# Performance work log

Hardware: AMD Instinct MI355X
Metric: run time of the kernel (lower is better)

The kernel has to match this reference:

```python
import jax, jax.numpy as jnp
import numpy as np

B, S, D, H, L, O = 64, 512, 512, 1024, 2, 1000


def setup_inputs() -> dict:
    key = jax.random.key(0)
    ks = jax.random.split(key, 12)
    s = 0.05
    return {
        "x": jax.random.normal(ks[0], (B, S, D), jnp.float32),
        "h0": jnp.zeros((L, B, H), jnp.float32),
        "c0": jnp.zeros((L, B, H), jnp.float32),
        "W_ih0": jax.random.normal(ks[1], (4 * H, D), jnp.float32) * s,
        "W_hh0": jax.random.normal(ks[2], (4 * H, H), jnp.float32) * s,
        "b_ih0": jax.random.normal(ks[3], (4 * H,), jnp.float32) * s,
        "b_hh0": jax.random.normal(ks[4], (4 * H,), jnp.float32) * s,
        "W_ih1": jax.random.normal(ks[5], (4 * H, H), jnp.float32) * s,
        "W_hh1": jax.random.normal(ks[6], (4 * H, H), jnp.float32) * s,
        "b_ih1": jax.random.normal(ks[7], (4 * H,), jnp.float32) * s,
        "b_hh1": jax.random.normal(ks[8], (4 * H,), jnp.float32) * s,
        "W_fc": jax.random.normal(ks[9], (O, H), jnp.float32) * s,
        "b_fc": jax.random.normal(ks[10], (O,), jnp.float32) * s,
    }


def _lstm_cell(x_t, h, c, W_ih, W_hh, b_ih, b_hh):
    # standard LSTMCell: fused 4-gate GEMM, gate order (i, f, g, o)
    gates = x_t @ W_ih.T + b_ih + h @ W_hh.T + b_hh  # [B, 4H]
    i, f, g, o = jnp.split(gates, 4, axis=-1)
    i = jax.nn.sigmoid(i)
    f = jax.nn.sigmoid(f)
    g = jnp.tanh(g)
    o = jax.nn.sigmoid(o)
    c_new = f * c + i * g
    h_new = o * jnp.tanh(c_new)
    return h_new, c_new


def reference(x, h0, c0, W_ih0, W_hh0, b_ih0, b_hh0, W_ih1, W_hh1, b_ih1, b_hh1, W_fc, b_fc):
    params = [(W_ih0, W_hh0, b_ih0, b_hh0), (W_ih1, W_hh1, b_ih1, b_hh1)]

    def step(carry, x_t):
        hs, cs = carry  # tuples of [B,H] per layer
        new_h, new_c = [], []
        inp = x_t
        for l in range(L):  # fixed small layer count
            h_l, c_l = _lstm_cell(inp, hs[l], cs[l], *params[l])
            new_h.append(h_l)
            new_c.append(c_l)
            inp = h_l
        return (tuple(new_h), tuple(new_c)), None

    xs = jnp.swapaxes(x, 0, 1)  # [S, B, D]
    init = (tuple(h0[l] for l in range(L)), tuple(c0[l] for l in range(L)))
    (hs, _), _ = jax.lax.scan(step, init, xs)
    # dropout is inference-mode identity; output_activation=None
    out = hs[-1] @ W_fc.T + b_fc  # [B, O]
    return out
```

## Files before the change

kernel.cpp:

```cpp
#include <hip/hip_runtime.h>

#define B_ 64
#define S_ 512
#define D_ 512
#define H_ 1024

typedef __attribute__((ext_vector_type(8))) short bf16x8;
typedef __attribute__((ext_vector_type(4))) float f32x4;
typedef unsigned short u16;
typedef unsigned int u32;

#define MFMA(a, b, c) __builtin_amdgcn_mfma_f32_16x16x32_bf16(a, b, c, 0, 0, 0)

__device__ __forceinline__ u16 f2bf(float f) {
    u32 u = __float_as_uint(f);
    u += 0x7fffu + ((u >> 16) & 1u);
    return (u16)(u >> 16);
}
__device__ __forceinline__ float sigm(float x) { return 1.0f / (1.0f + __expf(-x)); }
__device__ __forceinline__ float tanh_f(float x) { return 1.0f - 2.0f / (__expf(2.0f * x) + 1.0f); }

__device__ __forceinline__ bf16x8 cvt8(const float* p) {
    float4 f0 = ((const float4*)p)[0];
    float4 f1 = ((const float4*)p)[1];
    bf16x8 v;
    v[0] = (short)f2bf(f0.x); v[1] = (short)f2bf(f0.y);
    v[2] = (short)f2bf(f0.z); v[3] = (short)f2bf(f0.w);
    v[4] = (short)f2bf(f1.x); v[5] = (short)f2bf(f1.y);
    v[6] = (short)f2bf(f1.z); v[7] = (short)f2bf(f1.w);
    return v;
}

__device__ __forceinline__ void llc_ld(bf16x8& d, const u16* p) {
    asm volatile("global_load_dwordx4 %0, %1, off sc0 sc1" : "=v"(d) : "v"(p));
}
__device__ __forceinline__ void vm0() {
    asm volatile("s_waitcnt vmcnt(0)" ::: "memory");
}
__device__ __forceinline__ void fence_frag(bf16x8& d) {
    asm volatile("" : "+v"(d));
}
__device__ __forceinline__ void llc_st16(u16* p, u16 v) {
    u32 vv = v;
    asm volatile("global_store_short %0, %1, off sc0 sc1" :: "v"(p), "v"(vv) : "memory");
}

__global__ void prep_w(const float* __restrict__ Wih, const float* __restrict__ Whh,
                       u16* __restrict__ Wc, int Kx, int Kw, int total8) {
    int idx = blockIdx.x * 256 + threadIdx.x;
    if (idx >= total8) return;
    int kc8 = Kw >> 3;
    int n = idx / kc8;
    int kc = (idx - n * kc8) << 3;
    const float* src = (kc < Kx) ? (Wih + (size_t)n * Kx + kc)
                                 : (Whh + (size_t)n * (Kw - Kx) + (kc - Kx));
    *(bf16x8*)(Wc + (size_t)n * Kw + kc) = cvt8(src);
}

__global__ void prep_misc2(const float* __restrict__ h0in,
                           const float* __restrict__ bih0, const float* __restrict__ bhh0,
                           const float* __restrict__ bih1, const float* __restrict__ bhh1,
                           float* __restrict__ bias0, float* __restrict__ bias1,
                           u16* __restrict__ h0a, u16* __restrict__ h0b,
                           u16* __restrict__ h1a, u16* __restrict__ h1b,
                           int* __restrict__ bar) {
    int idx = blockIdx.x * 256 + threadIdx.x;
    if (idx < 1024) bar[idx] = 0;
    if (idx < 4096) { bias0[idx] = bih0[idx] + bhh0[idx]; return; }
    if (idx < 8192) { int i = idx - 4096; bias1[i] = bih1[i] + bhh1[i]; return; }
    int r = idx - 8192;
    if (r >= 2 * B_ * H_) return;
    int l = r >> 16;
    int rr = r & 65535;
    u16 hb = f2bf(h0in[r]);
    if (l == 0) { h0a[rr] = hb; h0b[rr] = hb; }
    else        { h1a[rr] = hb; h1b[rr] = hb; }
}

__global__ __launch_bounds__(512, 2) void lstm_persist(
    const float* __restrict__ x,
    const u16* __restrict__ W0c, const u16* __restrict__ W1c,
    const float* __restrict__ bias0, const float* __restrict__ bias1,
    const float* __restrict__ c0in,
    u16* __restrict__ h0a, u16* __restrict__ h0b,
    u16* __restrict__ h1a, u16* __restrict__ h1b,
    float* __restrict__ h1f,
    int* __restrict__ bar) {
    const int bk = blockIdx.x;
    const int cgp = bk >> 1;
    const int mh = bk & 1;
    const int tid = threadIdx.x;
    const int w = tid >> 6;
    const int lane = tid & 63;
    const int quad = lane >> 4;
    const int l16 = lane & 15;

    int gc[2];
    #pragma unroll
    for (int n = 0; n < 2; ++n) {
        int c = n * 16 + l16;
        gc[n] = (c >> 3) * 1024 + cgp * 8 + (c & 7);
    }

    bf16x8 w0x[2][2], w0h[2][4];
    bf16x8 w1f[2][8];
    #pragma unroll
    for (int n = 0; n < 2; ++n) {
        #pragma unroll
        for (int kf = 0; kf < 2; ++kf)
            w0x[n][kf] = *(const bf16x8*)(W0c + (size_t)gc[n] * 1536 + w * 64 + kf * 32 + quad * 8);
        #pragma unroll
        for (int kf = 0; kf < 4; ++kf)
            w0h[n][kf] = *(const bf16x8*)(W0c + (size_t)gc[n] * 1536 + 512 + w * 128 + kf * 32 + quad * 8);
        #pragma unroll
        for (int kf = 0; kf < 8; ++kf)
            w1f[n][kf] = *(const bf16x8*)(W1c + (size_t)gc[n] * 2048 + w * 256 + kf * 32 + quad * 8);
    }

    __shared__ float part[8 * 32 * 37];
    __shared__ float c0l[256], c1l[256];
    __shared__ float b0l[32], b1l[32];

    if (tid < 32) {
        int gg = tid >> 3, j = tid & 7;
        b0l[tid] = bias0[gg * 1024 + cgp * 8 + j];
        b1l[tid] = bias1[gg * 1024 + cgp * 8 + j];
    }
    if (tid < 256) {
        int b = tid >> 3, j = tid & 7;
        int gi = (mh * 32 + b) * 1024 + cgp * 8 + j;
        c0l[tid] = c0in[gi];
        c1l[tid] = c0in[65536 + gi];
    }
    __syncthreads();

    const int brow0 = mh * 32 + l16;
    const int brow1 = brow0 + 16;

    f32x4 xacc[2][2];
    #define XPART(t)                                                                 \
        {                                                                            \
            xacc[0][0] = (f32x4){0.f,0.f,0.f,0.f}; xacc[0][1] = (f32x4){0.f,0.f,0.f,0.f}; \
            xacc[1][0] = (f32x4){0.f,0.f,0.f,0.f}; xacc[1][1] = (f32x4){0.f,0.f,0.f,0.f}; \
            _Pragma("unroll")                                                        \
            for (int kf = 0; kf < 2; ++kf) {                                         \
                int k = w * 64 + kf * 32 + quad * 8;                                 \
                bf16x8 a0 = cvt8(x + (size_t)brow0 * 262144 + (t) * 512 + k);        \
                bf16x8 a1 = cvt8(x + (size_t)brow1 * 262144 + (t) * 512 + k);        \
                xacc[0][0] = MFMA(a0, w0x[0][kf], xacc[0][0]);                       \
                xacc[0][1] = MFMA(a0, w0x[1][kf], xacc[0][1]);                       \
                xacc[1][0] = MFMA(a1, w0x[0][kf], xacc[1][0]);                       \
                xacc[1][1] = MFMA(a1, w0x[1][kf], xacc[1][1]);                       \
            }                                                                        \
        }

    XPART(0);

    for (int p = 0; p <= S_; ++p) {
        const int rd = p & 1;
        const u16* h0r = rd ? h0b : h0a;
        u16*       h0w_ = rd ? h0a : h0b;
        const u16* h1r = rd ? h1b : h1a;
        u16*       h1w_ = rd ? h1a : h1b;

        if (p > 0) {
            if (tid == 0) {
                int target = 256 * p;
                for (int it = 0; it < 20000; ++it) {
                    if (__hip_atomic_load(&bar[0], __ATOMIC_RELAXED, __HIP_MEMORY_SCOPE_AGENT) >= target)
                        break;
                    __builtin_amdgcn_s_sleep(1);
                }
            }
            __syncthreads();
        }

        bf16x8 a0[4], a1[4];
        if (p < S_) {
            #pragma unroll
            for (int kf = 0; kf < 4; ++kf) {
                int ko = w * 128 + kf * 32 + quad * 8;
                llc_ld(a0[kf], h0r + brow0 * 1024 + ko);
                llc_ld(a1[kf], h0r + brow1 * 1024 + ko);
            }
            vm0();
            #pragma unroll
            for (int kf = 0; kf < 4; ++kf) { fence_frag(a0[kf]); fence_frag(a1[kf]); }
        }
        bf16x8 pb0[8], pb1[8];
        if (p >= 1) {
            #pragma unroll
            for (int kf = 0; kf < 8; ++kf) {
                int k = w * 256 + kf * 32;
                const u16* src = (k < 1024) ? h0r : h1r;
                int ko = (k & 1023) + quad * 8;
                llc_ld(pb0[kf], src + brow0 * 1024 + ko);
                llc_ld(pb1[kf], src + brow1 * 1024 + ko);
            }
        }

        if (p < S_) {
            f32x4 acc00 = xacc[0][0], acc01 = xacc[0][1];
            f32x4 acc10 = xacc[1][0], acc11 = xacc[1][1];
            #pragma unroll
            for (int kf = 0; kf < 4; ++kf) {
                acc00 = MFMA(a0[kf], w0h[0][kf], acc00);
                acc01 = MFMA(a0[kf], w0h[1][kf], acc01);
                acc10 = MFMA(a1[kf], w0h[0][kf], acc10);
                acc11 = MFMA(a1[kf], w0h[1][kf], acc11);
            }
            #pragma unroll
            for (int r = 0; r < 4; ++r) {
                int r0 = quad * 4 + r, r1 = 16 + quad * 4 + r;
                part[w * 1184 + r0 * 37 + l16]      = acc00[r];
                part[w * 1184 + r0 * 37 + 16 + l16] = acc01[r];
                part[w * 1184 + r1 * 37 + l16]      = acc10[r];
                part[w * 1184 + r1 * 37 + 16 + l16] = acc11[r];
            }
            __syncthreads();
            if (tid < 256) {
                int b = tid >> 3, j = tid & 7;
                float g4[4];
                #pragma unroll
                for (int gg = 0; gg < 4; ++gg) {
                    float s = b0l[gg * 8 + j];
                    #pragma unroll
                    for (int w8 = 0; w8 < 8; ++w8)
                        s += part[w8 * 1184 + b * 37 + gg * 8 + j];
                    g4[gg] = s;
                }
                float c = c0l[tid];
                float cn = sigm(g4[1]) * c + sigm(g4[0]) * tanh_f(g4[2]);
                float hn = sigm(g4[3]) * tanh_f(cn);
                c0l[tid] = cn;
                llc_st16(h0w_ + (mh * 32 + b) * 1024 + cgp * 8 + j, f2bf(hn));
            }
            __syncthreads();
        }

        if (p >= 1) {
            vm0();
            #pragma unroll
            for (int kf = 0; kf < 8; ++kf) { fence_frag(pb0[kf]); fence_frag(pb1[kf]); }
            f32x4 acc00 = {0.f,0.f,0.f,0.f}, acc01 = {0.f,0.f,0.f,0.f};
            f32x4 acc10 = {0.f,0.f,0.f,0.f}, acc11 = {0.f,0.f,0.f,0.f};
            #pragma unroll
            for (int kf = 0; kf < 8; ++kf) {
                acc00 = MFMA(pb0[kf], w1f[0][kf], acc00);
                acc01 = MFMA(pb0[kf], w1f[1][kf], acc01);
                acc10 = MFMA(pb1[kf], w1f[0][kf], acc10);
                acc11 = MFMA(pb1[kf], w1f[1][kf], acc11);
            }
            #pragma unroll
            for (int r = 0; r < 4; ++r) {
                int r0 = quad * 4 + r, r1 = 16 + quad * 4 + r;
                part[w * 1184 + r0 * 37 + l16]      = acc00[r];
                part[w * 1184 + r0 * 37 + 16 + l16] = acc01[r];
                part[w * 1184 + r1 * 37 + l16]      = acc10[r];
                part[w * 1184 + r1 * 37 + 16 + l16] = acc11[r];
            }
            __syncthreads();
            if (tid < 256) {
                int b = tid >> 3, j = tid & 7;
                float g4[4];
                #pragma unroll
                for (int gg = 0; gg < 4; ++gg) {
                    float s = b1l[gg * 8 + j];
                    #pragma unroll
                    for (int w8 = 0; w8 < 8; ++w8)
                        s += part[w8 * 1184 + b * 37 + gg * 8 + j];
                    g4[gg] = s;
                }
                float c = c1l[tid];
                float cn = sigm(g4[1]) * c + sigm(g4[0]) * tanh_f(g4[2]);
                float hn = sigm(g4[3]) * tanh_f(cn);
                c1l[tid] = cn;
                int gi = (mh * 32 + b) * 1024 + cgp * 8 + j;
                llc_st16(h1w_ + gi, f2bf(hn));
                if (p == S_) h1f[gi] = hn;
            }
            __syncthreads();
        }

        if (p < S_) {
            if (tid == 0)
                __hip_atomic_fetch_add(&bar[0], 1, __ATOMIC_RELAXED, __HIP_MEMORY_SCOPE_AGENT);
            if (p + 1 < S_) XPART(p + 1);
        }
    }
}

__global__ void fc_k(const float* __restrict__ h1f, const float* __restrict__ Wfc,
                     const float* __restrict__ bfc, float* __restrict__ out) {
    int idx = blockIdx.x * 256 + threadIdx.x;
    if (idx >= 64 * 1000) return;
    int o = idx % 1000;
    int b = idx / 1000;
    const float4* hr = (const float4*)(h1f + b * H_);
    const float4* wr = (const float4*)(Wfc + (size_t)o * H_);
    float s = 0.f;
    #pragma unroll 4
    for (int k = 0; k < 256; ++k) {
        float4 a = hr[k];
        float4 w = wr[k];
        s += a.x * w.x + a.y * w.y + a.z * w.z + a.w * w.w;
    }
    out[idx] = s + bfc[o];
}

extern "C" void kernel_launch(void* const* d_in, const int* in_sizes, int n_in,
                              void* d_out, int out_size, void* d_ws, size_t ws_size,
                              hipStream_t stream) {
    const float* x    = (const float*)d_in[0];
    const float* h0in = (const float*)d_in[1];
    const float* c0in = (const float*)d_in[2];
    const float* Wih0 = (const float*)d_in[3];
    const float* Whh0 = (const float*)d_in[4];
    const float* bih0 = (const float*)d_in[5];
    const float* bhh0 = (const float*)d_in[6];
    const float* Wih1 = (const float*)d_in[7];
    const float* Whh1 = (const float*)d_in[8];
    const float* bih1 = (const float*)d_in[9];
    const float* bhh1 = (const float*)d_in[10];
    const float* Wfc  = (const float*)d_in[11];
    const float* bfc  = (const float*)d_in[12];
    float* out = (float*)d_out;

    char* ws = (char*)d_ws;
    size_t off = 0;
    auto alloc = [&](size_t bytes) {
        void* p = ws + off;
        off += (bytes + 255) & ~(size_t)255;
        return p;
    };
    u16* W0c   = (u16*)alloc((size_t)4096 * 1536 * 2);
    u16* W1c   = (u16*)alloc((size_t)4096 * 2048 * 2);
    float* bias0 = (float*)alloc(4096 * 4);
    float* bias1 = (float*)alloc(4096 * 4);
    u16* h0A   = (u16*)alloc(B_ * H_ * 2);
    u16* h0B   = (u16*)alloc(B_ * H_ * 2);
    u16* h1A   = (u16*)alloc(B_ * H_ * 2);
    u16* h1B   = (u16*)alloc(B_ * H_ * 2);
    float* h1f = (float*)alloc(B_ * H_ * 4);
    int* bar   = (int*)alloc(4096);

    prep_w<<<786432 / 256, 256, 0, stream>>>(Wih0, Whh0, W0c, 512, 1536, 786432);
    prep_w<<<1048576 / 256, 256, 0, stream>>>(Wih1, Whh1, W1c, 1024, 2048, 1048576);
    prep_misc2<<<(8192 + 2 * B_ * H_ + 255) / 256, 256, 0, stream>>>(
        h0in, bih0, bhh0, bih1, bhh1, bias0, bias1, h0A, h0B, h1A, h1B, bar);

    void* args[] = {(void*)&x, (void*)&W0c, (void*)&W1c, (void*)&bias0, (void*)&bias1,
                    (void*)&c0in, (void*)&h0A, (void*)&h0B, (void*)&h1A, (void*)&h1B,
                    (void*)&h1f, (void*)&bar};
    hipLaunchCooperativeKernel((void*)lstm_persist, dim3(256), dim3(512), args, 0, stream);

    fc_k<<<(64000 + 255) / 256, 256, 0, stream>>>(h1f, Wfc, bfc, out);
}
```

Before: 5.886 ms.

## Replace global atomic barrier with per-block flags and overlap layer phases

Replaces the single global atomic counter barrier with per-block step flags: each block writes its own flag and waits only on the flags of the producer blocks it reads from, polled by a whole wavefront. The layer-0 and layer-1 gate reductions get separate shared buffers, which drops a couple of __syncthreads per step, and the h loads for both layers are waited on together with vmcnt. The shared-memory layout is changed so the gate reduction reads float4 vectors, with bias stored gate-interleaved. The goal is lower per-step synchronization latency across the 512 sequential steps. The risks are ordering and visibility bugs in the flag protocol and correctness of the partial vmcnt wait.

```diff
diff --git a/kernel.cpp b/kernel.cpp
--- a/kernel.cpp
+++ b/kernel.cpp
@@ -37,12 +37,24 @@
 __device__ __forceinline__ void vm0() {
     asm volatile("s_waitcnt vmcnt(0)" ::: "memory");
 }
+__device__ __forceinline__ void vmw16() {
+    asm volatile("s_waitcnt vmcnt(16)" ::: "memory");
+}
 __device__ __forceinline__ void fence_frag(bf16x8& d) {
     asm volatile("" : "+v"(d));
 }
 __device__ __forceinline__ void llc_st16(u16* p, u16 v) {
     u32 vv = v;
     asm volatile("global_store_short %0, %1, off sc0 sc1" :: "v"(p), "v"(vv) : "memory");
+}
+__device__ __forceinline__ void llc_st32(int* p, int v) {
+    asm volatile("global_store_dword %0, %1, off sc0 sc1" :: "v"(p), "v"(v) : "memory");
+}
+__device__ __forceinline__ void llc_ld2(int& a, int& b, const int* p0, const int* p1) {
+    asm volatile("global_load_dword %0, %2, off sc0 sc1\n"
+                 "global_load_dword %1, %3, off sc0 sc1\n"
+                 "s_waitcnt vmcnt(0)"
+                 : "=&v"(a), "=&v"(b) : "v"(p0), "v"(p1) : "memory");
 }
 
 __global__ void prep_w(const float* __restrict__ Wih, const float* __restrict__ Whh,
@@ -65,7 +77,7 @@
                            u16* __restrict__ h1a, u16* __restrict__ h1b,
                            int* __restrict__ bar) {
     int idx = blockIdx.x * 256 + threadIdx.x;
-    if (idx < 1024) bar[idx] = 0;
+    if (idx < 8192) bar[idx] = 0;
     if (idx < 4096) { bias0[idx] = bih0[idx] + bhh0[idx]; return; }
     if (idx < 8192) { int i = idx - 4096; bias1[i] = bih1[i] + bhh1[i]; return; }
     int r = idx - 8192;
@@ -117,14 +129,15 @@
             w1f[n][kf] = *(const bf16x8*)(W1c + (size_t)gc[n] * 2048 + w * 256 + kf * 32 + quad * 8);
     }
 
-    __shared__ float part[8 * 32 * 37];
+    __shared__ __align__(16) float partA[8 * 32 * 36];
+    __shared__ __align__(16) float partB[8 * 32 * 36];
     __shared__ float c0l[256], c1l[256];
-    __shared__ float b0l[32], b1l[32];
+    __shared__ __align__(16) float b0l[32], b1l[32];
 
     if (tid < 32) {
         int gg = tid >> 3, j = tid & 7;
-        b0l[tid] = bias0[gg * 1024 + cgp * 8 + j];
-        b1l[tid] = bias1[gg * 1024 + cgp * 8 + j];
+        b0l[j * 4 + gg] = bias0[gg * 1024 + cgp * 8 + j];
+        b1l[j * 4 + gg] = bias1[gg * 1024 + cgp * 8 + j];
     }
     if (tid < 256) {
         int b = tid >> 3, j = tid & 7;
@@ -136,6 +149,11 @@
 
     const int brow0 = mh * 32 + l16;
     const int brow1 = brow0 + 16;
+
+    const int* q0 = bar + (2 * lane + mh) * 32;
+    const int* q1 = bar + (2 * (lane + 64) + mh) * 32;
+    const int co0 = (l16 & 7) * 4 + (l16 >> 3);
+    const int co1 = co0 + 2;
 
     f32x4 xacc[2][2];
     #define XPART(t)                                                                 \
@@ -164,18 +182,14 @@
         u16*       h1w_ = rd ? h1a : h1b;
 
         if (p > 0) {
-            if (tid == 0) {
-                int target = 256 * p;
-                for (int it = 0; it < 20000; ++it) {
-                    if (__hip_atomic_load(&bar[0], __ATOMIC_RELAXED, __HIP_MEMORY_SCOPE_AGENT) >= target)
-                        break;
-                    __builtin_amdgcn_s_sleep(1);
-                }
-            }
-            __syncthreads();
-        }
-
-        bf16x8 a0[4], a1[4];
+            int f0, f1;
+            for (int it = 0; it < 40000; ++it) {
+                llc_ld2(f0, f1, q0, q1);
+                if (__all((f0 >= p) && (f1 >= p))) break;
+            }
+        }
+
+        bf16x8 a0[4], a1[4], pb0[8], pb1[8];
         if (p < S_) {
             #pragma unroll
             for (int kf = 0; kf < 4; ++kf) {
@@ -183,11 +197,7 @@
                 llc_ld(a0[kf], h0r + brow0 * 1024 + ko);
                 llc_ld(a1[kf], h0r + brow1 * 1024 + ko);
             }
-            vm0();
-            #pragma unroll
-            for (int kf = 0; kf < 4; ++kf) { fence_frag(a0[kf]); fence_frag(a1[kf]); }
-        }
-        bf16x8 pb0[8], pb1[8];
+        }
         if (p >= 1) {
             #pragma unroll
             for (int kf = 0; kf < 8; ++kf) {
@@ -200,6 +210,9 @@
         }
 
         if (p < S_) {
+            if (p >= 1) vmw16(); else vm0();
+            #pragma unroll
+            for (int kf = 0; kf < 4; ++kf) { fence_frag(a0[kf]); fence_frag(a1[kf]); }
             f32x4 acc00 = xacc[0][0], acc01 = xacc[0][1];
             f32x4 acc10 = xacc[1][0], acc11 = xacc[1][1];
             #pragma unroll
@@ -211,37 +224,35 @@
             }
             #pragma unroll
             for (int r = 0; r < 4; ++r) {
-                int r0 = quad * 4 + r, r1 = 16 + quad * 4 + r;
-                part[w * 1184 + r0 * 37 + l16]      = acc00[r];
-                part[w * 1184 + r0 * 37 + 16 + l16] = acc01[r];
-                part[w * 1184 + r1 * 37 + l16]      = acc10[r];
-                part[w * 1184 + r1 * 37 + 16 + l16] = acc11[r];
-            }
-            __syncthreads();
-            if (tid < 256) {
-                int b = tid >> 3, j = tid & 7;
-                float g4[4];
-                #pragma unroll
-                for (int gg = 0; gg < 4; ++gg) {
-                    float s = b0l[gg * 8 + j];
-                    #pragma unroll
-                    for (int w8 = 0; w8 < 8; ++w8)
-                        s += part[w8 * 1184 + b * 37 + gg * 8 + j];
-                    g4[gg] = s;
-                }
-                float c = c0l[tid];
-                float cn = sigm(g4[1]) * c + sigm(g4[0]) * tanh_f(g4[2]);
-                float hn = sigm(g4[3]) * tanh_f(cn);
-                c0l[tid] = cn;
-                llc_st16(h0w_ + (mh * 32 + b) * 1024 + cgp * 8 + j, f2bf(hn));
-            }
-            __syncthreads();
-        }
+                int b0 = quad * 4 + r, b1 = b0 + 16;
+                partA[w * 1152 + b0 * 36 + co0] = acc00[r];
+                partA[w * 1152 + b0 * 36 + co1] = acc01[r];
+                partA[w * 1152 + b1 * 36 + co0] = acc10[r];
+                partA[w * 1152 + b1 * 36 + co1] = acc11[r];
+            }
+        }
+        __syncthreads();
 
         if (p >= 1) {
             vm0();
             #pragma unroll
             for (int kf = 0; kf < 8; ++kf) { fence_frag(pb0[kf]); fence_frag(pb1[kf]); }
+        }
+
+        if (p < S_ && tid < 256) {
+            int b = tid >> 3, j = tid & 7;
+            f32x4 s = *(const f32x4*)&b0l[j * 4];
+            #pragma unroll
+            for (int w8 = 0; w8 < 8; ++w8)
+                s += *(const f32x4*)&partA[w8 * 1152 + b * 36 + j * 4];
+            float c = c0l[tid];
+            float cn = sigm(s[1]) * c + sigm(s[0]) * tanh_f(s[2]);
+            float hn = sigm(s[3]) * tanh_f(cn);
+            c0l[tid] = cn;
+            llc_st16(h0w_ + (mh * 32 + b) * 1024 + cgp * 8 + j, f2bf(hn));
+        }
+
+        if (p >= 1) {
             f32x4 acc00 = {0.f,0.f,0.f,0.f}, acc01 = {0.f,0.f,0.f,0.f};
             f32x4 acc10 = {0.f,0.f,0.f,0.f}, acc11 = {0.f,0.f,0.f,0.f};
             #pragma unroll
@@ -253,38 +264,33 @@
             }
             #pragma unroll
             for (int r = 0; r < 4; ++r) {
-                int r0 = quad * 4 + r, r1 = 16 + quad * 4 + r;
-                part[w * 1184 + r0 * 37 + l16]      = acc00[r];
-                part[w * 1184 + r0 * 37 + 16 + l16] = acc01[r];
-                part[w * 1184 + r1 * 37 + l16]      = acc10[r];
-                part[w * 1184 + r1 * 37 + 16 + l16] = acc11[r];
-            }
+                int b0 = quad * 4 + r, b1 = b0 + 16;
+                partB[w * 1152 + b0 * 36 + co0] = acc00[r];
+                partB[w * 1152 + b0 * 36 + co1] = acc01[r];
+                partB[w * 1152 + b1 * 36 + co0] = acc10[r];
+                partB[w * 1152 + b1 * 36 + co1] = acc11[r];
+            }
+        }
+        __syncthreads();
+        if (p >= 1 && tid < 256) {
+            int b = tid >> 3, j = tid & 7;
+            f32x4 s = *(const f32x4*)&b1l[j * 4];
+            #pragma unroll
+            for (int w8 = 0; w8 < 8; ++w8)
+                s += *(const f32x4*)&partB[w8 * 1152 + b * 36 + j * 4];
+            float c = c1l[tid];
+            float cn = sigm(s[1]) * c + sigm(s[0]) * tanh_f(s[2]);
+            float hn = sigm(s[3]) * tanh_f(cn);
+            c1l[tid] = cn;
+            int gi = (mh * 32 + b) * 1024 + cgp * 8 + j;
+            llc_st16(h1w_ + gi, f2bf(hn));
+            if (p == S_) h1f[gi] = hn;
+        }
+
+        if (p < S_) {
+            vm0();
             __syncthreads();
-            if (tid < 256) {
-                int b = tid >> 3, j = tid & 7;
-                float g4[4];
-                #pragma unroll
-                for (int gg = 0; gg < 4; ++gg) {
-                    float s = b1l[gg * 8 + j];
-                    #pragma unroll
-                    for (int w8 = 0; w8 < 8; ++w8)
-                        s += part[w8 * 1184 + b * 37 + gg * 8 + j];
-                    g4[gg] = s;
-                }
-                float c = c1l[tid];
-                float cn = sigm(g4[1]) * c + sigm(g4[0]) * tanh_f(g4[2]);
-                float hn = sigm(g4[3]) * tanh_f(cn);
-                c1l[tid] = cn;
-                int gi = (mh * 32 + b) * 1024 + cgp * 8 + j;
-                llc_st16(h1w_ + gi, f2bf(hn));
-                if (p == S_) h1f[gi] = hn;
-            }
-            __syncthreads();
-        }
-
-        if (p < S_) {
-            if (tid == 0)
-                __hip_atomic_fetch_add(&bar[0], 1, __ATOMIC_RELAXED, __HIP_MEMORY_SCOPE_AGENT);
+            if (tid == 0) llc_st32(bar + bk * 32, p + 1);
             if (p + 1 < S_) XPART(p + 1);
         }
     }
@@ -342,7 +348,7 @@
     u16* h1A   = (u16*)alloc(B_ * H_ * 2);
     u16* h1B   = (u16*)alloc(B_ * H_ * 2);
     float* h1f = (float*)alloc(B_ * H_ * 4);
-    int* bar   = (int*)alloc(4096);
+    int* bar   = (int*)alloc(32768);
 
     prep_w<<<786432 / 256, 256, 0, stream>>>(Wih0, Whh0, W0c, 512, 1536, 786432);
     prep_w<<<1048576 / 256, 256, 0, stream>>>(Wih1, Whh1, W1c, 1024, 2048, 1048576);
```

After: 6.250 ms. 1.06x slower.
